# Kernel optimization log

Measured on AMD Instinct MI355X. Metric: run time of the kernel, lower is better.

## Reference

```python
import jax, jax.numpy as jnp
import numpy as np

B, SE, HD, ED, N, T = 64, 512, 1024, 512, 10000, 20
EOS_ID = 1
NEG_BIG = -1e9    # stand-in for -MAX_VAL encoder pad mask
MASK_VAL = -1e7   # logits_mask scatter value (-10000000.0 in torch)
M = HD + ED


def setup_inputs() -> dict:
    key = jax.random.key(0)
    ks = jax.random.split(key, 16)
    s = 0.02
    enc = jax.random.normal(ks[0], (B, SE, HD), jnp.float32)
    hidden = jax.random.normal(ks[1], (1, B, HD), jnp.float32)
    cell = jax.random.normal(ks[2], (1, B, HD), jnp.float32)
    text_lengths = jax.random.randint(ks[3], (B,), SE // 2, SE + 1)
    encoder_mask = jnp.arange(SE)[None, :] < text_lengths[:, None]  # [B,SE] bool
    embedding = jax.random.normal(ks[4], (N, ED), jnp.float32) * s
    # LSTM (PyTorch gate order i,f,g,o)
    w_ih = jax.random.normal(ks[5], (4 * HD, ED), jnp.float32) * s
    w_hh = jax.random.normal(ks[6], (4 * HD, HD), jnp.float32) * s
    b_ih = jnp.zeros((4 * HD,), jnp.float32)
    b_hh = jnp.zeros((4 * HD,), jnp.float32)
    # dense_net: Hd -> He
    w_q = jax.random.normal(ks[7], (HD, HD), jnp.float32) * s
    b_q = jnp.zeros((HD,), jnp.float32)
    # SelfAttentiveSum: Linear(Ed,Ed)+ReLU+Linear(Ed,1)
    w_k = jax.random.normal(ks[8], (ED, ED), jnp.float32) * s
    b_k = jnp.zeros((ED,), jnp.float32)
    w_ko = jax.random.normal(ks[9], (ED,), jnp.float32) * s
    b_ko = jnp.zeros((), jnp.float32)
    # MLP: Linear(M,M)+ReLU+Linear(M,N)
    w_m1 = jax.random.normal(ks[10], (M, M), jnp.float32) * s
    b_m1 = jnp.zeros((M,), jnp.float32)
    w_m2 = jax.random.normal(ks[11], (N, M), jnp.float32) * s
    b_m2 = jnp.zeros((N,), jnp.float32)
    return dict(encoded_hidden_embeddings=enc, hidden=hidden, cell=cell,
                text_lengths=text_lengths, encoder_mask=encoder_mask,
                embedding=embedding, w_ih=w_ih, w_hh=w_hh, b_ih=b_ih, b_hh=b_hh,
                w_q=w_q, b_q=b_q, w_k=w_k, b_k=b_k, w_ko=w_ko, b_ko=b_ko,
                w_m1=w_m1, b_m1=b_m1, w_m2=w_m2, b_m2=b_m2)


def _decode(enc, h0, c0, encoder_mask, embedding, w_ih, w_hh, b_ih, b_hh,
            w_q, b_q, w_k, b_k, w_ko, b_ko, w_m1, b_m1, w_m2, b_m2):
    pad_mask = jnp.where(encoder_mask, 0.0, NEG_BIG).astype(enc.dtype)  # [B,SE]
    sent = enc[:, 0, :]  # [B,HD] sentence representation (dropout is identity in eval)

    def step(carry, t):
        h, c, inp, logits_mask, buf = carry
        # --- LSTM cell (single step) ---
        gates = inp @ w_ih.T + b_ih + h @ w_hh.T + b_hh  # [B,4HD]
        i, f, g, o = jnp.split(gates, 4, axis=-1)
        c = jax.nn.sigmoid(f) * c + jax.nn.sigmoid(i) * jnp.tanh(g)
        h = jax.nn.sigmoid(o) * jnp.tanh(c)
        # --- attention over encoder states ---
        q = h @ w_q.T + b_q                                   # [B,HD]
        score = jnp.einsum('bsh,bh->bs', enc, q) + pad_mask    # [B,SE]
        w = jax.nn.softmax(score, axis=1)
        attn_enc = jnp.einsum('bs,bsh->bh', w, enc)            # [B,HD]
        # --- self-attentive sum over previously predicted label embeddings ---
        valid = jnp.arange(T) < jnp.maximum(t, 1)              # step 0: zeros row 0 valid
        k = jax.nn.relu(buf @ w_k.T + b_k) @ w_ko + b_ko       # [B,T]
        k = jnp.where(valid[None, :], k, NEG_BIG)
        sw = jax.nn.softmax(k, axis=1)
        attn_last = jnp.einsum('bt,bte->be', sw, buf)          # [B,ED]
        # --- MLP ---
        m = jnp.concatenate([sent + attn_enc, inp + attn_last], axis=-1)  # [B,M]
        logits = jax.nn.relu(m @ w_m1.T + b_m1) @ w_m2.T + b_m2 + logits_mask  # [B,N]
        next_ids = jnp.argmax(logits, axis=-1)                 # [B]
        pred_emb = embedding[next_ids]                          # [B,ED]
        buf = buf.at[:, t].set(pred_emb)
        logits_mask = logits_mask.at[jnp.arange(B), next_ids].set(MASK_VAL)
        logits_mask = logits_mask.at[:, EOS_ID].set(0.0)
        return (h, c, pred_emb, logits_mask, buf), (logits, next_ids)

    init = (h0, c0,
            jnp.zeros((B, ED), enc.dtype),
            jnp.zeros((B, N), enc.dtype),
            jnp.zeros((B, T, ED), enc.dtype))
    _, (outs, ids) = jax.lax.scan(step, init, jnp.arange(T))
    return jnp.transpose(outs, (1, 0, 2)), jnp.transpose(ids, (1, 0))  # [B,T,N],[B,T]


def reference(encoded_hidden_embeddings, hidden, cell, text_lengths, encoder_mask,
              embedding, w_ih, w_hh, b_ih, b_hh, w_q, b_q, w_k, b_k, w_ko, b_ko,
              w_m1, b_m1, w_m2, b_m2):
    # De=1: [1,B,HD] -> [B,HD]
    return _decode(encoded_hidden_embeddings, hidden[0], cell[0], encoder_mask,
                   embedding, w_ih, w_hh, b_ih, b_hh, w_q, b_q, w_k, b_k,
                   w_ko, b_ko, w_m1, b_m1, w_m2, b_m2)
```

## Files before the change

kernel.cpp:

```cpp
#include <hip/hip_runtime.h>

#define B64 64
#define SE 512
#define HD 1024
#define ED 512
#define NV 10000
#define TT 20
#define MM 1536
#define MASK_VALF -10000000.0f

#define OFF_XT    0
#define OFF_CT    98304
#define OFF_A     163840
#define OFF_B     4003840
#define OFF_QF    5052416
#define OFF_FM    5117952
#define OFF_FL    5118976
#define OFF_XT2   5120000
#define OFF_H1T   5218304
#define OFF_ARGV  5316608
#define OFF_ARGI  5396608
#define OFF_MASKT 5476608
#define OFF_BUF   6116608
#define OFF_BUFT  6771968
#define OFF_KVP   7427328

__device__ __forceinline__ float sigmoidf_(float x) { return 1.f / (1.f + expf(-x)); }

__global__ __launch_bounds__(256) void k_init(const float* __restrict__ h0,
                                              const float* __restrict__ c0,
                                              float* __restrict__ ws) {
  int idx = blockIdx.x * 256 + threadIdx.x, stride = gridDim.x * 256;
  float* inpT = ws + OFF_XT;
  float* hT = ws + OFF_XT + 512 * 64;
  float* cT = ws + OFF_CT;
  float* maskT = ws + OFF_MASKT;
  float* buf = ws + OFF_BUF;
  float* bufT = ws + OFF_BUFT;
  for (int i = idx; i < 512 * 64; i += stride) inpT[i] = 0.f;
  for (int i = idx; i < NV * 64; i += stride) maskT[i] = 0.f;
  for (int i = idx; i < B64 * TT * ED; i += stride) { buf[i] = 0.f; bufT[i] = 0.f; }
  for (int i = idx; i < HD * 64; i += stride) {
    int u = i >> 6, b = i & 63;
    hT[i] = h0[b * HD + u];
    cT[i] = c0[b * HD + u];
  }
}

template <int KT>
__global__ __launch_bounds__(256) void k_gemm(const float* __restrict__ W, int ldW,
                                              const float* __restrict__ x,
                                              float* __restrict__ part, int nrows, size_t psz) {
  __shared__ float wl[32][KT];
  int tid = threadIdx.x;
  int r0b = blockIdx.x * 32;
  int split = blockIdx.y;
  int k0 = split * KT;
  constexpr int NF4 = 32 * KT / 4;
  for (int i = tid; i < NF4; i += 256) {
    int r = i / (KT / 4), kk = (i % (KT / 4)) * 4;
    int gr = r0b + r;
    if (gr > nrows - 1) gr = nrows - 1;
    *(float4*)&wl[r][kk] = *(const float4*)&W[(size_t)gr * ldW + k0 + kk];
  }
  __syncthreads();
  int lane = tid & 63, wid = tid >> 6;
  const float* xp = x + (size_t)k0 * 64 + lane;
  float acc[8] = {0, 0, 0, 0, 0, 0, 0, 0};
#pragma unroll 2
  for (int k4 = 0; k4 < KT / 4; ++k4) {
    float x0 = xp[(4 * k4 + 0) * 64];
    float x1 = xp[(4 * k4 + 1) * 64];
    float x2 = xp[(4 * k4 + 2) * 64];
    float x3 = xp[(4 * k4 + 3) * 64];
#pragma unroll
    for (int i = 0; i < 8; ++i) {
      const float4 w4 = *(const float4*)&wl[wid * 8 + i][4 * k4];
      acc[i] = fmaf(w4.x, x0, acc[i]);
      acc[i] = fmaf(w4.y, x1, acc[i]);
      acc[i] = fmaf(w4.z, x2, acc[i]);
      acc[i] = fmaf(w4.w, x3, acc[i]);
    }
  }
  int r0 = r0b + wid * 8;
  float* o = part + (size_t)split * psz + (size_t)r0 * 64 + lane;
#pragma unroll
  for (int i = 0; i < 8; ++i)
    if (r0 + i < nrows) o[i * 64] = acc[i];
}

__global__ __launch_bounds__(256) void k_gates(const float* __restrict__ xt,
                                               const float* __restrict__ w_ih,
                                               const float* __restrict__ w_hh,
                                               float* __restrict__ gpart) {
  __shared__ float wl[32][256];
  int tid = threadIdx.x;
  int r0b = blockIdx.x * 32;
  int y = blockIdx.y;
  const float* W;
  int ldW, k0, xoff;
  if (y < 2) { W = w_ih; ldW = 512; k0 = y * 256; xoff = k0; }
  else { W = w_hh; ldW = 1024; k0 = (y - 2) * 256; xoff = 512 + k0; }
  for (int i = tid; i < 32 * 64; i += 256) {
    int r = i >> 6, kk = (i & 63) * 4;
    *(float4*)&wl[r][kk] = *(const float4*)&W[(size_t)(r0b + r) * ldW + k0 + kk];
  }
  __syncthreads();
  int lane = tid & 63, wid = tid >> 6;
  const float* xp = xt + (size_t)xoff * 64 + lane;
  float acc[8] = {0, 0, 0, 0, 0, 0, 0, 0};
#pragma unroll 2
  for (int k4 = 0; k4 < 64; ++k4) {
    float x0 = xp[(4 * k4 + 0) * 64];
    float x1 = xp[(4 * k4 + 1) * 64];
    float x2 = xp[(4 * k4 + 2) * 64];
    float x3 = xp[(4 * k4 + 3) * 64];
#pragma unroll
    for (int i = 0; i < 8; ++i) {
      const float4 w4 = *(const float4*)&wl[wid * 8 + i][4 * k4];
      acc[i] = fmaf(w4.x, x0, acc[i]);
      acc[i] = fmaf(w4.y, x1, acc[i]);
      acc[i] = fmaf(w4.z, x2, acc[i]);
      acc[i] = fmaf(w4.w, x3, acc[i]);
    }
  }
  int r0 = r0b + wid * 8;
  float* o = gpart + ((size_t)y * 262144 + (size_t)r0 * 64) + lane;
#pragma unroll
  for (int i = 0; i < 8; ++i) o[i * 64] = acc[i];
}

__global__ __launch_bounds__(256) void k_lstm(const float* __restrict__ gpart,
                                              const float* __restrict__ b_ih,
                                              const float* __restrict__ b_hh,
                                              float* __restrict__ cT, float* __restrict__ hT) {
  int i = blockIdx.x * 256 + threadIdx.x;
  int u = i >> 6, b = i & 63;
  float g4[4];
#pragma unroll
  for (int gi = 0; gi < 4; ++gi) {
    int r = gi * 1024 + u;
    float v = b_ih[r] + b_hh[r];
#pragma unroll
    for (int y = 0; y < 6; ++y) v += gpart[(size_t)y * 262144 + (size_t)r * 64 + b];
    g4[gi] = v;
  }
  float c = cT[i];
  float cn = sigmoidf_(g4[1]) * c + sigmoidf_(g4[0]) * tanhf(g4[2]);
  float hn = sigmoidf_(g4[3]) * tanhf(cn);
  cT[i] = cn;
  hT[i] = hn;
}

__global__ __launch_bounds__(256) void k_qfin(const float* __restrict__ qpart,
                                              const float* __restrict__ b_q,
                                              float* __restrict__ qf) {
  __shared__ float tile[64][65];
  int h0 = blockIdx.x * 64;
  int lane = threadIdx.x & 63, hrow = threadIdx.x >> 6;
#pragma unroll
  for (int p = 0; p < 16; ++p) {
    int hl = p * 4 + hrow;
    int h = h0 + hl;
    float v = b_q[h];
#pragma unroll
    for (int s = 0; s < 8; ++s) v += qpart[((size_t)s * 1024 + h) * 64 + lane];
    tile[hl][lane] = v;
  }
  __syncthreads();
#pragma unroll
  for (int p = 0; p < 16; ++p) {
    int b = p * 4 + hrow;
    qf[(size_t)b * 1024 + h0 + lane] = tile[lane][b];
  }
}

__global__ __launch_bounds__(256) void k_flash(const float* __restrict__ enc,
                                               const int* __restrict__ tlen,
                                               const float* __restrict__ qf,
                                               float* __restrict__ fm, float* __restrict__ fl,
                                               float* __restrict__ facc) {
  __shared__ float lacc[4][1024];
  __shared__ float lml[4][2];
  int b = blockIdx.x >> 4, split = blockIdx.x & 15;
  int tid = threadIdx.x, lane = tid & 63, wid = tid >> 6;
  int len = tlen[b];
  float qv[16];
#pragma unroll
  for (int j = 0; j < 4; ++j) {
    float4 tq = *(const float4*)&qf[(size_t)b * 1024 + j * 256 + lane * 4];
    qv[4 * j + 0] = tq.x; qv[4 * j + 1] = tq.y; qv[4 * j + 2] = tq.z; qv[4 * j + 3] = tq.w;
  }
  const float* base = enc + (size_t)b * SE * HD;
  int s0 = split * 32 + wid * 8;
  int nr = len - s0;
  nr = nr < 0 ? 0 : (nr > 8 ? 8 : nr);
  int npair = nr >> 1;

  float4 cA[4], cB[4], nA[4], nB[4];
  float m = -1e30f, l = 0.f, acc[16];
#pragma unroll
  for (int j = 0; j < 16; ++j) acc[j] = 0.f;

#define LOADROW(d, s)                                            \
  {                                                              \
    const float4* rp = (const float4*)(base + (size_t)(s)*HD) + lane; \
    d[0] = rp[0]; d[1] = rp[64]; d[2] = rp[128]; d[3] = rp[192]; \
  }

  if (npair > 0) { LOADROW(cA, s0); LOADROW(cB, s0 + 1); }
  for (int p = 0; p < npair; ++p) {
    if (p + 1 < npair) {
      LOADROW(nA, s0 + 2 * p + 2);
      LOADROW(nB, s0 + 2 * p + 3);
    } else if (nr & 1) {
      LOADROW(nA, s0 + nr - 1);
    }
    float d0 = 0.f, d1 = 0.f;
#pragma unroll
    for (int j = 0; j < 4; ++j) {
      d0 = fmaf(qv[4 * j + 0], cA[j].x, d0); d1 = fmaf(qv[4 * j + 0], cB[j].x, d1);
      d0 = fmaf(qv[4 * j + 1], cA[j].y, d0); d1 = fmaf(qv[4 * j + 1], cB[j].y, d1);
      d0 = fmaf(qv[4 * j + 2], cA[j].z, d0); d1 = fmaf(qv[4 * j + 2], cB[j].z, d1);
      d0 = fmaf(qv[4 * j + 3], cA[j].w, d0); d1 = fmaf(qv[4 * j + 3], cB[j].w, d1);
    }
#pragma unroll
    for (int off = 32; off; off >>= 1) { d0 += __shfl_xor(d0, off, 64); d1 += __shfl_xor(d1, off, 64); }
    d0 = __shfl(d0, 0, 64);
    d1 = __shfl(d1, 0, 64);
    float mn = fmaxf(m, fmaxf(d0, d1));
    float sc = expf(m - mn), p0 = expf(d0 - mn), p1 = expf(d1 - mn);
    l = l * sc + p0 + p1;
#pragma unroll
    for (int j = 0; j < 4; ++j) {
      acc[4 * j + 0] = fmaf(p1, cB[j].x, fmaf(p0, cA[j].x, acc[4 * j + 0] * sc));
      acc[4 * j + 1] = fmaf(p1, cB[j].y, fmaf(p0, cA[j].y, acc[4 * j + 1] * sc));
      acc[4 * j + 2] = fmaf(p1, cB[j].z, fmaf(p0, cA[j].z, acc[4 * j + 2] * sc));
      acc[4 * j + 3] = fmaf(p1, cB[j].w, fmaf(p0, cA[j].w, acc[4 * j + 3] * sc));
    }
    m = mn;
#pragma unroll
    for (int j = 0; j < 4; ++j) { cA[j] = nA[j]; cB[j] = nB[j]; }
  }
  if (nr & 1) {
    if (npair == 0) LOADROW(cA, s0);
    float d0 = 0.f;
#pragma unroll
    for (int j = 0; j < 4; ++j) {
      d0 = fmaf(qv[4 * j + 0], cA[j].x, d0);
      d0 = fmaf(qv[4 * j + 1], cA[j].y, d0);
      d0 = fmaf(qv[4 * j + 2], cA[j].z, d0);
      d0 = fmaf(qv[4 * j + 3], cA[j].w, d0);
    }
#pragma unroll
    for (int off = 32; off; off >>= 1) d0 += __shfl_xor(d0, off, 64);
    d0 = __shfl(d0, 0, 64);
    float mn = fmaxf(m, d0);
    float sc = expf(m - mn), p0 = expf(d0 - mn);
    l = l * sc + p0;
#pragma unroll
    for (int j = 0; j < 4; ++j) {
      acc[4 * j + 0] = fmaf(p0, cA[j].x, acc[4 * j + 0] * sc);
      acc[4 * j + 1] = fmaf(p0, cA[j].y, acc[4 * j + 1] * sc);
      acc[4 * j + 2] = fmaf(p0, cA[j].z, acc[4 * j + 2] * sc);
      acc[4 * j + 3] = fmaf(p0, cA[j].w, acc[4 * j + 3] * sc);
    }
    m = mn;
  }
#undef LOADROW
#pragma unroll
  for (int j = 0; j < 4; ++j)
    *(float4*)&lacc[wid][j * 256 + lane * 4] =
        make_float4(acc[4 * j], acc[4 * j + 1], acc[4 * j + 2], acc[4 * j + 3]);
  if (lane == 0) { lml[wid][0] = m; lml[wid][1] = l; }
  __syncthreads();
  float M = fmaxf(fmaxf(lml[0][0], lml[1][0]), fmaxf(lml[2][0], lml[3][0]));
  float w0 = expf(lml[0][0] - M), w1 = expf(lml[1][0] - M);
  float w2 = expf(lml[2][0] - M), w3 = expf(lml[3][0] - M);
  float L = w0 * lml[0][1] + w1 * lml[1][1] + w2 * lml[2][1] + w3 * lml[3][1];
  int p = b * 16 + split;
  for (int h = tid; h < 1024; h += 256)
    facc[(size_t)p * 1024 + h] =
        w0 * lacc[0][h] + w1 * lacc[1][h] + w2 * lacc[2][h] + w3 * lacc[3][h];
  if (tid == 0) { fm[p] = M; fl[p] = L; }
}

__global__ __launch_bounds__(256) void k_ctx(const float* __restrict__ enc,
                                             const float* __restrict__ fm,
                                             const float* __restrict__ fl,
                                             const float* __restrict__ facc,
                                             const float* __restrict__ kvp,
                                             const float* __restrict__ b_ko,
                                             const float* __restrict__ buf,
                                             const float* __restrict__ inpT,
                                             float* __restrict__ xT2, int tv) {
  __shared__ float pw[TT];
  int b = blockIdx.x, tid = threadIdx.x;
  if (tid < tv) {
    float s = b_ko[0];
    for (int g = 0; g < 64; ++g) s += kvp[((size_t)g * TT + tid) * 64 + b];
    pw[tid] = s;
  }
  __syncthreads();
  float mx = -1e30f;
  for (int k = 0; k < tv; ++k) mx = fmaxf(mx, pw[k]);
  float den = 0.f;
  for (int k = 0; k < tv; ++k) den += expf(pw[k] - mx);
  float invd = 1.f / den;
  __syncthreads();
  if (tid < tv) pw[tid] = expf(pw[tid] - mx) * invd;
  __syncthreads();
  float M = -1e30f;
#pragma unroll
  for (int k = 0; k < 16; ++k) M = fmaxf(M, fm[b * 16 + k]);
  float w[16];
  float L = 0.f;
#pragma unroll
  for (int k = 0; k < 16; ++k) {
    w[k] = expf(fm[b * 16 + k] - M);
    L += w[k] * fl[b * 16 + k];
  }
  float inv = 1.f / L;
  for (int h = tid; h < 1024; h += 256) {
    float s = 0.f;
#pragma unroll
    for (int k = 0; k < 16; ++k) s += w[k] * facc[(size_t)(b * 16 + k) * 1024 + h];
    xT2[h * 64 + b] = enc[(size_t)b * SE * HD + h] + s * inv;
  }
  for (int e = tid; e < 512; e += 256) {
    float a = 0.f;
    for (int k = 0; k < tv; ++k) a += pw[k] * buf[((size_t)b * TT + k) * 512 + e];
    xT2[(1024 + e) * 64 + b] = inpT[e * 64 + b] + a;
  }
}

__global__ __launch_bounds__(256) void k_kscore(const float* __restrict__ bufT,
                                                const float* __restrict__ w_k,
                                                const float* __restrict__ b_k,
                                                const float* __restrict__ w_ko,
                                                float* __restrict__ kvp, int j) {
  __shared__ float sacc[4][8][64];
  int lane = threadIdx.x & 63, wid = threadIdx.x >> 6;
  int ug = blockIdx.x;
  int u0 = ug * 8;
  int k0 = wid * 128;
  const float* xp = bufT + (size_t)j * 64 + lane;
  float acc[8] = {0, 0, 0, 0, 0, 0, 0, 0};
  for (int k4 = 0; k4 < 32; ++k4) {
    int e = k0 + 4 * k4;
    float x0 = xp[(size_t)(e + 0) * (TT * 64)];
    float x1 = xp[(size_t)(e + 1) * (TT * 64)];
    float x2 = xp[(size_t)(e + 2) * (TT * 64)];
    float x3 = xp[(size_t)(e + 3) * (TT * 64)];
#pragma unroll
    for (int i = 0; i < 8; ++i) {
      const float4 w4 = *(const float4*)&w_k[(size_t)(u0 + i) * 512 + e];
      acc[i] = fmaf(w4.x, x0, acc[i]);
      acc[i] = fmaf(w4.y, x1, acc[i]);
      acc[i] = fmaf(w4.z, x2, acc[i]);
      acc[i] = fmaf(w4.w, x3, acc[i]);
    }
  }
#pragma unroll
  for (int i = 0; i < 8; ++i) sacc[wid][i][lane] = acc[i];
  __syncthreads();
  if (wid == 0) {
    float kp = 0.f;
#pragma unroll
    for (int i = 0; i < 8; ++i) {
      float tot = b_k[u0 + i] + sacc[0][i][lane] + sacc[1][i][lane] + sacc[2][i][lane] +
                  sacc[3][i][lane];
      kp += fmaxf(tot, 0.f) * w_ko[u0 + i];
    }
    kvp[((size_t)ug * TT + j) * 64 + lane] = kp;
  }
}

__global__ __launch_bounds__(256) void k_h1comb(const float* __restrict__ h1part,
                                                const float* __restrict__ b_m1,
                                                float* __restrict__ h1T) {
  int i = blockIdx.x * 256 + threadIdx.x;
  int r = i >> 6;
  float v = b_m1[r];
#pragma unroll
  for (int s = 0; s < 12; ++s) v += h1part[(size_t)s * 98304 + i];
  h1T[i] = fmaxf(v, 0.f);
}

__global__ __launch_bounds__(256) void k_logfin(const float* __restrict__ lp,
                                                const float* __restrict__ b_m2,
                                                const float* __restrict__ maskT,
                                                float* __restrict__ argv, int* __restrict__ argi,
                                                float* __restrict__ out, int t) {
  __shared__ float tile[32][65];
  int lane = threadIdx.x & 63, wid = threadIdx.x >> 6;
  int rg = blockIdx.x * 4 + wid;
  int nb = blockIdx.x * 32;
  if (rg < 1250) {
    int r0 = rg * 8;
    float best = -3.4e38f;
    int bi = 0;
#pragma unroll
    for (int i = 0; i < 8; ++i) {
      int r = r0 + i;
      size_t idx = (size_t)r * 64 + lane;
      float v = b_m2[r] + maskT[idx];
#pragma unroll
      for (int s = 0; s < 6; ++s) v += lp[(size_t)s * 640000 + idx];
      tile[wid * 8 + i][lane] = v;
      if (v > best) { best = v; bi = r; }
    }
    argv[(size_t)rg * 64 + lane] = best;
    argi[(size_t)rg * 64 + lane] = bi;
  }
  __syncthreads();
  int b = threadIdx.x >> 2, q = threadIdx.x & 3;
  int nloc = q * 8;
  if (nb + nloc < NV) {
    float tmp[8];
#pragma unroll
    for (int c = 0; c < 8; ++c) tmp[c] = tile[nloc + c][b];
    float4* o = (float4*)&out[((size_t)b * TT + t) * NV + nb + nloc];
    o[0] = make_float4(tmp[0], tmp[1], tmp[2], tmp[3]);
    o[1] = make_float4(tmp[4], tmp[5], tmp[6], tmp[7]);
  }
}

__global__ __launch_bounds__(256) void k_final(const float* __restrict__ argv,
                                               const int* __restrict__ argi,
                                               const float* __restrict__ emb,
                                               float* __restrict__ maskT, float* __restrict__ inpT,
                                               float* __restrict__ buf, float* __restrict__ bufT,
                                               float* __restrict__ out_ids, int t) {
  __shared__ float sv[256];
  __shared__ int si_[256];
  __shared__ int sid;
  int b = blockIdx.x, tid = threadIdx.x;
  float best = -3.4e38f;
  int bi = 0x7fffffff;
  for (int g = tid; g < 1250; g += 256) {
    float v = argv[(size_t)g * 64 + b];
    int idx = argi[(size_t)g * 64 + b];
    if (v > best || (v == best && idx < bi)) { best = v; bi = idx; }
  }
  sv[tid] = best;
  si_[tid] = bi;
  __syncthreads();
  for (int off = 128; off; off >>= 1) {
    if (tid < off) {
      float v2 = sv[tid + off];
      int i2 = si_[tid + off];
      if (v2 > sv[tid] || (v2 == sv[tid] && i2 < si_[tid])) { sv[tid] = v2; si_[tid] = i2; }
    }
    __syncthreads();
  }
  if (tid == 0) {
    sid = si_[0];
    out_ids[b * TT + t] = (float)si_[0];
    if (si_[0] != 1) maskT[(size_t)si_[0] * 64 + b] = MASK_VALF;
  }
  __syncthreads();
  int id = sid;
  for (int e = tid; e < 512; e += 256) {
    float v = emb[(size_t)id * 512 + e];
    inpT[e * 64 + b] = v;
    buf[((size_t)b * TT + t) * 512 + e] = v;
    bufT[(size_t)e * (TT * 64) + t * 64 + b] = v;
  }
}

extern "C" void kernel_launch(void* const* d_in, const int* in_sizes, int n_in,
                              void* d_out, int out_size, void* d_ws, size_t ws_size,
                              hipStream_t stream) {
  const float* enc = (const float*)d_in[0];
  const float* h0 = (const float*)d_in[1];
  const float* c0 = (const float*)d_in[2];
  const int* tlen = (const int*)d_in[3];
  const float* emb = (const float*)d_in[5];
  const float* w_ih = (const float*)d_in[6];
  const float* w_hh = (const float*)d_in[7];
  const float* b_ih = (const float*)d_in[8];
  const float* b_hh = (const float*)d_in[9];
  const float* w_q = (const float*)d_in[10];
  const float* b_q = (const float*)d_in[11];
  const float* w_k = (const float*)d_in[12];
  const float* b_k = (const float*)d_in[13];
  const float* w_ko = (const float*)d_in[14];
  const float* b_ko = (const float*)d_in[15];
  const float* w_m1 = (const float*)d_in[16];
  const float* b_m1 = (const float*)d_in[17];
  const float* w_m2 = (const float*)d_in[18];
  const float* b_m2 = (const float*)d_in[19];

  float* ws = (float*)d_ws;
  float* out_logits = (float*)d_out;
  float* out_ids = out_logits + (size_t)B64 * TT * NV;

  float* xt = ws + OFF_XT;
  float* hT = xt + 512 * 64;

  k_init<<<2048, 256, 0, stream>>>(h0, c0, ws);
  k_kscore<<<64, 256, 0, stream>>>(ws + OFF_BUFT, w_k, b_k, w_ko, ws + OFF_KVP, 0);

  for (int t = 0; t < TT; ++t) {
    int tv = (t < 1) ? 1 : t;
    k_gates<<<dim3(128, 6), 256, 0, stream>>>(xt, w_ih, w_hh, ws + OFF_A);
    k_lstm<<<256, 256, 0, stream>>>(ws + OFF_A, b_ih, b_hh, ws + OFF_CT, hT);
    k_gemm<128><<<dim3(32, 8), 256, 0, stream>>>(w_q, 1024, hT, ws + OFF_B, 1024, 65536);
    k_qfin<<<16, 256, 0, stream>>>(ws + OFF_B, b_q, ws + OFF_QF);
    k_flash<<<1024, 256, 0, stream>>>(enc, tlen, ws + OFF_QF, ws + OFF_FM, ws + OFF_FL,
                                      ws + OFF_B);
    k_ctx<<<64, 256, 0, stream>>>(enc, ws + OFF_FM, ws + OFF_FL, ws + OFF_B, ws + OFF_KVP, b_ko,
                                  ws + OFF_BUF, xt, ws + OFF_XT2, tv);
    k_gemm<128><<<dim3(48, 12), 256, 0, stream>>>(w_m1, MM, ws + OFF_XT2, ws + OFF_A, MM, 98304);
    k_h1comb<<<384, 256, 0, stream>>>(ws + OFF_A, b_m1, ws + OFF_H1T);
    k_gemm<256><<<dim3(313, 6), 256, 0, stream>>>(w_m2, MM, ws + OFF_H1T, ws + OFF_A, NV, 640000);
    k_logfin<<<313, 256, 0, stream>>>(ws + OFF_A, b_m2, ws + OFF_MASKT, ws + OFF_ARGV,
                                      (int*)(ws + OFF_ARGI), out_logits, t);
    k_final<<<64, 256, 0, stream>>>(ws + OFF_ARGV, (int*)(ws + OFF_ARGI), emb, ws + OFF_MASKT, xt,
                                    ws + OFF_BUF, ws + OFF_BUFT, out_ids, t);
    if (t < TT - 1)
      k_kscore<<<64, 256, 0, stream>>>(ws + OFF_BUFT, w_k, b_k, w_ko, ws + OFF_KVP, t);
  }
}
```

Measured before the change: 3.328 ms.

## Fuse LSTM gate GEMM with cell update and merge flash-attention with context reduction

Replaces the split-K gate GEMM and the separate LSTM pointwise kernel with one kernel. Each block computes all four gates for two hidden units over the full K and applies the cell update in place, ping-ponging h between two buffers. The flash-attention and context kernels are merged using an atomic counter, so the last of eight splits per batch row does the final reduction. Splits per batch drop from 16 to 8. This removes two launches and the partial-sum round trips per step, at the cost of less parallelism in the gate kernel and atomics plus threadfence ordering.

```diff
diff --git a/kernel.cpp b/kernel.cpp
--- a/kernel.cpp
+++ b/kernel.cpp
@@ -10,20 +10,23 @@
 #define MASK_VALF -10000000.0f
 
 #define OFF_XT    0
-#define OFF_CT    98304
-#define OFF_A     163840
-#define OFF_B     4003840
-#define OFF_QF    5052416
-#define OFF_FM    5117952
-#define OFF_FL    5118976
-#define OFF_XT2   5120000
-#define OFF_H1T   5218304
-#define OFF_ARGV  5316608
-#define OFF_ARGI  5396608
-#define OFF_MASKT 5476608
-#define OFF_BUF   6116608
-#define OFF_BUFT  6771968
-#define OFF_KVP   7427328
+#define OFF_HA    32768
+#define OFF_HB    98304
+#define OFF_CT    163840
+#define OFF_A     229376
+#define OFF_B     4069376
+#define OFF_QF    4593664
+#define OFF_FM    4659200
+#define OFF_FL    4659712
+#define OFF_XT2   4660224
+#define OFF_H1T   4758528
+#define OFF_ARGV  4856832
+#define OFF_ARGI  4936832
+#define OFF_MASKT 5016832
+#define OFF_BUF   5656832
+#define OFF_BUFT  6312192
+#define OFF_KVP   6967552
+#define OFF_CNT   7049472
 
 __device__ __forceinline__ float sigmoidf_(float x) { return 1.f / (1.f + expf(-x)); }
 
@@ -32,18 +35,102 @@
                                               float* __restrict__ ws) {
   int idx = blockIdx.x * 256 + threadIdx.x, stride = gridDim.x * 256;
   float* inpT = ws + OFF_XT;
-  float* hT = ws + OFF_XT + 512 * 64;
+  float* hA = ws + OFF_HA;
   float* cT = ws + OFF_CT;
   float* maskT = ws + OFF_MASKT;
   float* buf = ws + OFF_BUF;
   float* bufT = ws + OFF_BUFT;
+  int* cnt = (int*)(ws + OFF_CNT);
   for (int i = idx; i < 512 * 64; i += stride) inpT[i] = 0.f;
   for (int i = idx; i < NV * 64; i += stride) maskT[i] = 0.f;
   for (int i = idx; i < B64 * TT * ED; i += stride) { buf[i] = 0.f; bufT[i] = 0.f; }
   for (int i = idx; i < HD * 64; i += stride) {
     int u = i >> 6, b = i & 63;
-    hT[i] = h0[b * HD + u];
+    hA[i] = h0[b * HD + u];
     cT[i] = c0[b * HD + u];
+  }
+  if (idx < 64) cnt[idx] = 0;
+}
+
+__global__ __launch_bounds__(256) void k_cell(const float* __restrict__ inpT,
+                                              const float* __restrict__ h_in,
+                                              const float* __restrict__ w_ih,
+                                              const float* __restrict__ w_hh,
+                                              const float* __restrict__ b_ih,
+                                              const float* __restrict__ b_hh,
+                                              float* __restrict__ cT,
+                                              float* __restrict__ h_out) {
+  __shared__ float wl[8 * 1024];
+  __shared__ float ex[8][64];
+  int tid = threadIdx.x, lane = tid & 63, wid = tid >> 6;
+  int u0 = blockIdx.x * 2;
+  int r0 = wid * 1024 + u0;
+  float acc0 = b_ih[r0] + b_hh[r0];
+  float acc1 = b_ih[r0 + 1] + b_hh[r0 + 1];
+  for (int i = tid; i < 1024; i += 256) {
+    int rr = i >> 7, kk = (i & 127) * 4;
+    *(float4*)&wl[rr * 512 + kk] =
+        *(const float4*)&w_ih[(size_t)((rr >> 1) * 1024 + u0 + (rr & 1)) * 512 + kk];
+  }
+  __syncthreads();
+  {
+    const float* xp = inpT + lane;
+    const float* w0p = &wl[(wid * 2 + 0) * 512];
+    const float* w1p = &wl[(wid * 2 + 1) * 512];
+#pragma unroll 2
+    for (int k4 = 0; k4 < 128; ++k4) {
+      float x0 = xp[(4 * k4 + 0) * 64];
+      float x1 = xp[(4 * k4 + 1) * 64];
+      float x2 = xp[(4 * k4 + 2) * 64];
+      float x3 = xp[(4 * k4 + 3) * 64];
+      float4 wa = *(const float4*)&w0p[4 * k4];
+      float4 wb = *(const float4*)&w1p[4 * k4];
+      acc0 = fmaf(wa.x, x0, acc0); acc1 = fmaf(wb.x, x0, acc1);
+      acc0 = fmaf(wa.y, x1, acc0); acc1 = fmaf(wb.y, x1, acc1);
+      acc0 = fmaf(wa.z, x2, acc0); acc1 = fmaf(wb.z, x2, acc1);
+      acc0 = fmaf(wa.w, x3, acc0); acc1 = fmaf(wb.w, x3, acc1);
+    }
+  }
+  __syncthreads();
+  for (int i = tid; i < 2048; i += 256) {
+    int rr = i >> 8, kk = (i & 255) * 4;
+    *(float4*)&wl[rr * 1024 + kk] =
+        *(const float4*)&w_hh[(size_t)((rr >> 1) * 1024 + u0 + (rr & 1)) * 1024 + kk];
+  }
+  __syncthreads();
+  {
+    const float* xp = h_in + lane;
+    const float* w0p = &wl[(wid * 2 + 0) * 1024];
+    const float* w1p = &wl[(wid * 2 + 1) * 1024];
+#pragma unroll 2
+    for (int k4 = 0; k4 < 256; ++k4) {
+      float x0 = xp[(4 * k4 + 0) * 64];
+      float x1 = xp[(4 * k4 + 1) * 64];
+      float x2 = xp[(4 * k4 + 2) * 64];
+      float x3 = xp[(4 * k4 + 3) * 64];
+      float4 wa = *(const float4*)&w0p[4 * k4];
+      float4 wb = *(const float4*)&w1p[4 * k4];
+      acc0 = fmaf(wa.x, x0, acc0); acc1 = fmaf(wb.x, x0, acc1);
+      acc0 = fmaf(wa.y, x1, acc0); acc1 = fmaf(wb.y, x1, acc1);
+      acc0 = fmaf(wa.z, x2, acc0); acc1 = fmaf(wb.z, x2, acc1);
+      acc0 = fmaf(wa.w, x3, acc0); acc1 = fmaf(wb.w, x3, acc1);
+    }
+  }
+  ex[wid * 2 + 0][lane] = acc0;
+  ex[wid * 2 + 1][lane] = acc1;
+  __syncthreads();
+  if (tid < 128) {
+    int j = tid >> 6, b = tid & 63;
+    int u = u0 + j;
+    float gi = ex[0 + j][b];
+    float gf = ex[2 + j][b];
+    float gg = ex[4 + j][b];
+    float go = ex[6 + j][b];
+    float c = cT[u * 64 + b];
+    float cn = sigmoidf_(gf) * c + sigmoidf_(gi) * tanhf(gg);
+    float hn = sigmoidf_(go) * tanhf(cn);
+    cT[u * 64 + b] = cn;
+    h_out[u * 64 + b] = hn;
   }
 }
 
@@ -89,69 +176,6 @@
     if (r0 + i < nrows) o[i * 64] = acc[i];
 }
 
-__global__ __launch_bounds__(256) void k_gates(const float* __restrict__ xt,
-                                               const float* __restrict__ w_ih,
-                                               const float* __restrict__ w_hh,
-                                               float* __restrict__ gpart) {
-  __shared__ float wl[32][256];
-  int tid = threadIdx.x;
-  int r0b = blockIdx.x * 32;
-  int y = blockIdx.y;
-  const float* W;
-  int ldW, k0, xoff;
-  if (y < 2) { W = w_ih; ldW = 512; k0 = y * 256; xoff = k0; }
-  else { W = w_hh; ldW = 1024; k0 = (y - 2) * 256; xoff = 512 + k0; }
-  for (int i = tid; i < 32 * 64; i += 256) {
-    int r = i >> 6, kk = (i & 63) * 4;
-    *(float4*)&wl[r][kk] = *(const float4*)&W[(size_t)(r0b + r) * ldW + k0 + kk];
-  }
-  __syncthreads();
-  int lane = tid & 63, wid = tid >> 6;
-  const float* xp = xt + (size_t)xoff * 64 + lane;
-  float acc[8] = {0, 0, 0, 0, 0, 0, 0, 0};
-#pragma unroll 2
-  for (int k4 = 0; k4 < 64; ++k4) {
-    float x0 = xp[(4 * k4 + 0) * 64];
-    float x1 = xp[(4 * k4 + 1) * 64];
-    float x2 = xp[(4 * k4 + 2) * 64];
-    float x3 = xp[(4 * k4 + 3) * 64];
-#pragma unroll
-    for (int i = 0; i < 8; ++i) {
-      const float4 w4 = *(const float4*)&wl[wid * 8 + i][4 * k4];
-      acc[i] = fmaf(w4.x, x0, acc[i]);
-      acc[i] = fmaf(w4.y, x1, acc[i]);
-      acc[i] = fmaf(w4.z, x2, acc[i]);
-      acc[i] = fmaf(w4.w, x3, acc[i]);
-    }
-  }
-  int r0 = r0b + wid * 8;
-  float* o = gpart + ((size_t)y * 262144 + (size_t)r0 * 64) + lane;
-#pragma unroll
-  for (int i = 0; i < 8; ++i) o[i * 64] = acc[i];
-}
-
-__global__ __launch_bounds__(256) void k_lstm(const float* __restrict__ gpart,
-                                              const float* __restrict__ b_ih,
-                                              const float* __restrict__ b_hh,
-                                              float* __restrict__ cT, float* __restrict__ hT) {
-  int i = blockIdx.x * 256 + threadIdx.x;
-  int u = i >> 6, b = i & 63;
-  float g4[4];
-#pragma unroll
-  for (int gi = 0; gi < 4; ++gi) {
-    int r = gi * 1024 + u;
-    float v = b_ih[r] + b_hh[r];
-#pragma unroll
-    for (int y = 0; y < 6; ++y) v += gpart[(size_t)y * 262144 + (size_t)r * 64 + b];
-    g4[gi] = v;
-  }
-  float c = cT[i];
-  float cn = sigmoidf_(g4[1]) * c + sigmoidf_(g4[0]) * tanhf(g4[2]);
-  float hn = sigmoidf_(g4[3]) * tanhf(cn);
-  cT[i] = cn;
-  hT[i] = hn;
-}
-
 __global__ __launch_bounds__(256) void k_qfin(const float* __restrict__ qpart,
                                               const float* __restrict__ b_q,
                                               float* __restrict__ qf) {
@@ -175,14 +199,20 @@
   }
 }
 
-__global__ __launch_bounds__(256) void k_flash(const float* __restrict__ enc,
-                                               const int* __restrict__ tlen,
-                                               const float* __restrict__ qf,
-                                               float* __restrict__ fm, float* __restrict__ fl,
-                                               float* __restrict__ facc) {
+__global__ __launch_bounds__(256) void k_flashctx(const float* __restrict__ enc,
+                                                  const int* __restrict__ tlen,
+                                                  const float* __restrict__ qf,
+                                                  const float* __restrict__ kvp,
+                                                  const float* __restrict__ b_ko,
+                                                  const float* __restrict__ buf,
+                                                  const float* __restrict__ inpT,
+                                                  float* __restrict__ fm, float* __restrict__ fl,
+                                                  float* __restrict__ facc, int* __restrict__ cnt,
+                                                  float* __restrict__ xT2, int tv) {
   __shared__ float lacc[4][1024];
   __shared__ float lml[4][2];
-  int b = blockIdx.x >> 4, split = blockIdx.x & 15;
+  __shared__ int lastflag;
+  int b = blockIdx.x >> 3, split = blockIdx.x & 7;
   int tid = threadIdx.x, lane = tid & 63, wid = tid >> 6;
   int len = tlen[b];
   float qv[16];
@@ -192,9 +222,9 @@
     qv[4 * j + 0] = tq.x; qv[4 * j + 1] = tq.y; qv[4 * j + 2] = tq.z; qv[4 * j + 3] = tq.w;
   }
   const float* base = enc + (size_t)b * SE * HD;
-  int s0 = split * 32 + wid * 8;
+  int s0 = split * 64 + wid * 16;
   int nr = len - s0;
-  nr = nr < 0 ? 0 : (nr > 8 ? 8 : nr);
+  nr = nr < 0 ? 0 : (nr > 16 ? 16 : nr);
   int npair = nr >> 1;
 
   float4 cA[4], cB[4], nA[4], nB[4];
@@ -202,10 +232,10 @@
 #pragma unroll
   for (int j = 0; j < 16; ++j) acc[j] = 0.f;
 
-#define LOADROW(d, s)                                            \
-  {                                                              \
+#define LOADROW(d, s)                                                 \
+  {                                                                   \
     const float4* rp = (const float4*)(base + (size_t)(s)*HD) + lane; \
-    d[0] = rp[0]; d[1] = rp[64]; d[2] = rp[128]; d[3] = rp[192]; \
+    d[0] = rp[0]; d[1] = rp[64]; d[2] = rp[128]; d[3] = rp[192];      \
   }
 
   if (npair > 0) { LOADROW(cA, s0); LOADROW(cB, s0 + 1); }
@@ -274,28 +304,25 @@
         make_float4(acc[4 * j], acc[4 * j + 1], acc[4 * j + 2], acc[4 * j + 3]);
   if (lane == 0) { lml[wid][0] = m; lml[wid][1] = l; }
   __syncthreads();
-  float M = fmaxf(fmaxf(lml[0][0], lml[1][0]), fmaxf(lml[2][0], lml[3][0]));
-  float w0 = expf(lml[0][0] - M), w1 = expf(lml[1][0] - M);
-  float w2 = expf(lml[2][0] - M), w3 = expf(lml[3][0] - M);
-  float L = w0 * lml[0][1] + w1 * lml[1][1] + w2 * lml[2][1] + w3 * lml[3][1];
-  int p = b * 16 + split;
+  float M4 = fmaxf(fmaxf(lml[0][0], lml[1][0]), fmaxf(lml[2][0], lml[3][0]));
+  float w0 = expf(lml[0][0] - M4), w1 = expf(lml[1][0] - M4);
+  float w2 = expf(lml[2][0] - M4), w3 = expf(lml[3][0] - M4);
+  float L4 = w0 * lml[0][1] + w1 * lml[1][1] + w2 * lml[2][1] + w3 * lml[3][1];
+  int p = b * 8 + split;
   for (int h = tid; h < 1024; h += 256)
     facc[(size_t)p * 1024 + h] =
         w0 * lacc[0][h] + w1 * lacc[1][h] + w2 * lacc[2][h] + w3 * lacc[3][h];
-  if (tid == 0) { fm[p] = M; fl[p] = L; }
-}
-
-__global__ __launch_bounds__(256) void k_ctx(const float* __restrict__ enc,
-                                             const float* __restrict__ fm,
-                                             const float* __restrict__ fl,
-                                             const float* __restrict__ facc,
-                                             const float* __restrict__ kvp,
-                                             const float* __restrict__ b_ko,
-                                             const float* __restrict__ buf,
-                                             const float* __restrict__ inpT,
-                                             float* __restrict__ xT2, int tv) {
+  if (tid == 0) { fm[p] = M4; fl[p] = L4; }
+  __threadfence();
+  if (tid == 0) {
+    int old = atomicAdd(&cnt[b], 1);
+    lastflag = (old == 7);
+  }
+  __syncthreads();
+  if (!lastflag) return;
+  if (tid == 0) cnt[b] = 0;
+  __threadfence();
   __shared__ float pw[TT];
-  int b = blockIdx.x, tid = threadIdx.x;
   if (tid < tv) {
     float s = b_ko[0];
     for (int g = 0; g < 64; ++g) s += kvp[((size_t)g * TT + tid) * 64 + b];
@@ -312,19 +339,19 @@
   __syncthreads();
   float M = -1e30f;
 #pragma unroll
-  for (int k = 0; k < 16; ++k) M = fmaxf(M, fm[b * 16 + k]);
-  float w[16];
+  for (int k = 0; k < 8; ++k) M = fmaxf(M, fm[b * 8 + k]);
+  float w[8];
   float L = 0.f;
 #pragma unroll
-  for (int k = 0; k < 16; ++k) {
-    w[k] = expf(fm[b * 16 + k] - M);
-    L += w[k] * fl[b * 16 + k];
+  for (int k = 0; k < 8; ++k) {
+    w[k] = expf(fm[b * 8 + k] - M);
+    L += w[k] * fl[b * 8 + k];
   }
   float inv = 1.f / L;
   for (int h = tid; h < 1024; h += 256) {
     float s = 0.f;
 #pragma unroll
-    for (int k = 0; k < 16; ++k) s += w[k] * facc[(size_t)(b * 16 + k) * 1024 + h];
+    for (int k = 0; k < 8; ++k) s += w[k] * facc[(size_t)(b * 8 + k) * 1024 + h];
     xT2[h * 64 + b] = enc[(size_t)b * SE * HD + h] + s * inv;
   }
   for (int e = tid; e < 512; e += 256) {
@@ -496,29 +523,30 @@
   float* out_logits = (float*)d_out;
   float* out_ids = out_logits + (size_t)B64 * TT * NV;
 
-  float* xt = ws + OFF_XT;
-  float* hT = xt + 512 * 64;
+  float* inpT = ws + OFF_XT;
+  float* hA = ws + OFF_HA;
+  float* hB = ws + OFF_HB;
 
   k_init<<<2048, 256, 0, stream>>>(h0, c0, ws);
   k_kscore<<<64, 256, 0, stream>>>(ws + OFF_BUFT, w_k, b_k, w_ko, ws + OFF_KVP, 0);
 
   for (int t = 0; t < TT; ++t) {
     int tv = (t < 1) ? 1 : t;
-    k_gates<<<dim3(128, 6), 256, 0, stream>>>(xt, w_ih, w_hh, ws + OFF_A);
-    k_lstm<<<256, 256, 0, stream>>>(ws + OFF_A, b_ih, b_hh, ws + OFF_CT, hT);
-    k_gemm<128><<<dim3(32, 8), 256, 0, stream>>>(w_q, 1024, hT, ws + OFF_B, 1024, 65536);
+    float* h_in = (t & 1) ? hB : hA;
+    float* h_out = (t & 1) ? hA : hB;
+    k_cell<<<512, 256, 0, stream>>>(inpT, h_in, w_ih, w_hh, b_ih, b_hh, ws + OFF_CT, h_out);
+    k_gemm<128><<<dim3(32, 8), 256, 0, stream>>>(w_q, 1024, h_out, ws + OFF_B, 1024, 65536);
     k_qfin<<<16, 256, 0, stream>>>(ws + OFF_B, b_q, ws + OFF_QF);
-    k_flash<<<1024, 256, 0, stream>>>(enc, tlen, ws + OFF_QF, ws + OFF_FM, ws + OFF_FL,
-                                      ws + OFF_B);
-    k_ctx<<<64, 256, 0, stream>>>(enc, ws + OFF_FM, ws + OFF_FL, ws + OFF_B, ws + OFF_KVP, b_ko,
-                                  ws + OFF_BUF, xt, ws + OFF_XT2, tv);
+    k_flashctx<<<512, 256, 0, stream>>>(enc, tlen, ws + OFF_QF, ws + OFF_KVP, b_ko, ws + OFF_BUF,
+                                        inpT, ws + OFF_FM, ws + OFF_FL, ws + OFF_B,
+                                        (int*)(ws + OFF_CNT), ws + OFF_XT2, tv);
     k_gemm<128><<<dim3(48, 12), 256, 0, stream>>>(w_m1, MM, ws + OFF_XT2, ws + OFF_A, MM, 98304);
     k_h1comb<<<384, 256, 0, stream>>>(ws + OFF_A, b_m1, ws + OFF_H1T);
     k_gemm<256><<<dim3(313, 6), 256, 0, stream>>>(w_m2, MM, ws + OFF_H1T, ws + OFF_A, NV, 640000);
     k_logfin<<<313, 256, 0, stream>>>(ws + OFF_A, b_m2, ws + OFF_MASKT, ws + OFF_ARGV,
                                       (int*)(ws + OFF_ARGI), out_logits, t);
-    k_final<<<64, 256, 0, stream>>>(ws + OFF_ARGV, (int*)(ws + OFF_ARGI), emb, ws + OFF_MASKT, xt,
-                                    ws + OFF_BUF, ws + OFF_BUFT, out_ids, t);
+    k_final<<<64, 256, 0, stream>>>(ws + OFF_ARGV, (int*)(ws + OFF_ARGI), emb, ws + OFF_MASKT,
+                                    inpT, ws + OFF_BUF, ws + OFF_BUFT, out_ids, t);
     if (t < TT - 1)
       k_kscore<<<64, 256, 0, stream>>>(ws + OFF_BUFT, w_k, b_k, w_ko, ws + OFF_KVP, t);
   }
```

New measurement: 6.048 ms. 1.82x slower.
